# Performance work log

Hardware: AMD Instinct MI355X
Metric: run time of the kernel (lower is better)

The kernel has to match this reference:

```python
import jax, jax.numpy as jnp
import numpy as np

DIM, DEPTH, HEADS, MLP = 1024, 6, 16, 4096
HEAD_DIM = DIM // HEADS
SCALE = DIM ** -0.5  # NOTE: original uses full dim, not head_dim
EPS = 1e-5


def _layernorm(x, g, b):
    m = jnp.mean(x, axis=-1, keepdims=True)
    v = jnp.mean((x - m) ** 2, axis=-1, keepdims=True)
    return (x - m) * jax.lax.rsqrt(v + EPS) * g + b


def setup_inputs() -> dict:
    key = jax.random.key(0)
    ks = jax.random.split(key, 12)
    d = DEPTH
    s_qkv = (DIM * 3) ** -0.5  # ~kaiming-ish scale, values only need to be plausible
    inp = {
        "x": jax.random.normal(ks[0], (2, 2048, DIM), dtype=jnp.float32),
        "Wqkv": jax.random.normal(ks[1], (d, DIM, 3 * DIM), dtype=jnp.float32) * s_qkv,
        "Wout": jax.random.normal(ks[2], (d, DIM, DIM), dtype=jnp.float32) * (DIM ** -0.5),
        "bout": jnp.zeros((d, DIM), dtype=jnp.float32),
        "ln1_g": jnp.ones((d, DIM), dtype=jnp.float32),
        "ln1_b": jnp.zeros((d, DIM), dtype=jnp.float32),
        "ln2_g": jnp.ones((d, DIM), dtype=jnp.float32),
        "ln2_b": jnp.zeros((d, DIM), dtype=jnp.float32),
        "W1": jax.random.normal(ks[3], (d, DIM, MLP), dtype=jnp.float32) * (DIM ** -0.5),
        "b1": jnp.zeros((d, MLP), dtype=jnp.float32),
        "W2": jax.random.normal(ks[4], (d, MLP, DIM), dtype=jnp.float32) * (MLP ** -0.5),
        "b2": jnp.zeros((d, DIM), dtype=jnp.float32),
    }
    return inp


def _transformer(x, Wqkv, Wout, bout, ln1_g, ln1_b, ln2_g, ln2_b, W1, b1, W2, b2):
    b, n, _ = x.shape

    def layer(h, p):
        wqkv, wout, bo, g1, bb1, g2, bb2, w1, bf1, w2, bf2 = p
        # --- attention block (Residual(PreNorm(SelfAttention))) ---
        y = _layernorm(h, g1, bb1)
        qkv = y @ wqkv                                   # [b, n, 3*dim]
        qkv = qkv.reshape(b, n, 3, HEADS, HEAD_DIM)
        q, k, v = [jnp.transpose(qkv[:, :, i], (0, 2, 1, 3)) for i in range(3)]  # [b,h,n,d]
        dots = jnp.einsum("bhid,bhjd->bhij", q, k) * SCALE
        attn = jax.nn.softmax(dots, axis=-1)
        o = jnp.einsum("bhij,bhjd->bhid", attn, v)       # [b,h,n,d]
        o = jnp.transpose(o, (0, 2, 1, 3)).reshape(b, n, DIM)
        h = h + (o @ wout + bo)
        # --- FFN block (Residual(PreNorm(FeedForward))) ---
        y = _layernorm(h, g2, bb2)
        y = jax.nn.gelu(y @ w1 + bf1, approximate=False) @ w2 + bf2
        return h + y, None

    params = (Wqkv, Wout, bout, ln1_g, ln1_b, ln2_g, ln2_b, W1, b1, W2, b2)
    out, _ = jax.lax.scan(layer, x, params)
    return out


def reference(x, Wqkv, Wout, bout, ln1_g, ln1_b, ln2_g, ln2_b, W1, b1, W2, b2):
    return _transformer(x, Wqkv, Wout, bout, ln1_g, ln1_b, ln2_g, ln2_b, W1, b1, W2, b2)
```

## Files before the change

### kernel.cpp

```cpp
#include <hip/hip_runtime.h>
#include <hip/hip_bf16.h>
#include <math.h>

typedef __attribute__((__ext_vector_type__(8))) __bf16 bf16x8;
typedef __attribute__((__ext_vector_type__(4))) float f32x4;

#define DIMQ 1024
#define SEQ 2048
#define NTOK 4096
#define HEADS 16
#define HD 64
#define MLPD 4096
#define DEPTH 6

__device__ __forceinline__ void gl_lds16(const __hip_bfloat16* g, __hip_bfloat16* l) {
  __builtin_amdgcn_global_load_lds((const __attribute__((address_space(1))) void*)(g),
                                   (__attribute__((address_space(3))) void*)(l), 16, 0, 0);
}

__global__ __launch_bounds__(256) void ln_kernel(const float* __restrict__ h,
                                                 const float* __restrict__ g,
                                                 const float* __restrict__ bta,
                                                 __hip_bfloat16* __restrict__ y) {
  int row = blockIdx.x;
  int t = threadIdx.x;
  const float4* src = (const float4*)(h + (size_t)row * DIMQ);
  float4 xv = src[t];
  float s = xv.x + xv.y + xv.z + xv.w;
  float ss = xv.x * xv.x + xv.y * xv.y + xv.z * xv.z + xv.w * xv.w;
#pragma unroll
  for (int off = 32; off > 0; off >>= 1) {
    s += __shfl_xor(s, off);
    ss += __shfl_xor(ss, off);
  }
  __shared__ float red[8];
  int wid = t >> 6;
  if ((t & 63) == 0) { red[wid] = s; red[4 + wid] = ss; }
  __syncthreads();
  s = red[0] + red[1] + red[2] + red[3];
  ss = red[4] + red[5] + red[6] + red[7];
  float mean = s * (1.0f / DIMQ);
  float var = ss * (1.0f / DIMQ) - mean * mean;
  float rstd = rsqrtf(var + 1e-5f);
  float4 gv = ((const float4*)g)[t];
  float4 bv = ((const float4*)bta)[t];
  __hip_bfloat16* dst = y + (size_t)row * DIMQ + t * 4;
  dst[0] = __float2bfloat16((xv.x - mean) * rstd * gv.x + bv.x);
  dst[1] = __float2bfloat16((xv.y - mean) * rstd * gv.y + bv.y);
  dst[2] = __float2bfloat16((xv.z - mean) * rstd * gv.z + bv.z);
  dst[3] = __float2bfloat16((xv.w - mean) * rstd * gv.w + bv.w);
}

__global__ __launch_bounds__(256) void transpose_cast(const float* __restrict__ in,
                                                      __hip_bfloat16* __restrict__ out,
                                                      int K, int N) {
  __shared__ float t[32][33];
  int n0 = blockIdx.x * 32, k0 = blockIdx.y * 32;
  int tx = threadIdx.x, ty = threadIdx.y;
#pragma unroll
  for (int i = 0; i < 32; i += 8)
    t[ty + i][tx] = in[(size_t)(k0 + ty + i) * N + n0 + tx];
  __syncthreads();
#pragma unroll
  for (int i = 0; i < 32; i += 8)
    out[(size_t)(n0 + ty + i) * K + k0 + tx] = __float2bfloat16(t[tx][ty + i]);
}

__global__ __launch_bounds__(256) void vtrans(const __hip_bfloat16* __restrict__ qkvb,
                                              __hip_bfloat16* __restrict__ vT) {
  __shared__ __hip_bfloat16 t[32][33];
  int n0 = blockIdx.x * 32, d0 = blockIdx.y * 32, bh = blockIdx.z;
  int tx = threadIdx.x, ty = threadIdx.y;
#pragma unroll
  for (int i = 0; i < 32; i += 8)
    t[ty + i][tx] = qkvb[((size_t)(64 + bh) * SEQ + n0 + ty + i) * HD + d0 + tx];
  __syncthreads();
#pragma unroll
  for (int i = 0; i < 32; i += 8)
    vT[((size_t)bh * HD + d0 + ty + i) * SEQ + n0 + tx] = t[tx][ty + i];
}

template <int EPI>
__global__ __launch_bounds__(256)
void gemm128(const __hip_bfloat16* __restrict__ A, const __hip_bfloat16* __restrict__ BT,
             const float* __restrict__ bias, void* __restrict__ outp,
             int M, int N, int K, int gpx) {
  __shared__ __hip_bfloat16 As[128][64];
  __shared__ __hip_bfloat16 Bs[128][64];
  int bid = blockIdx.x;
  int xcd = bid & 7, jb = bid >> 3;
  int nt = xcd * gpx + (jb % gpx), mt = jb / gpx;
  int m0 = mt * 128, n0 = nt * 128;
  int tid = threadIdx.x;
  int lane = tid & 63, wid = tid >> 6;
  int l16 = lane & 15, quad = lane >> 4;
  int wm = (wid >> 1) * 64, wn = (wid & 1) * 64;
  int srsub = lane >> 3;
  int sg = (lane & 7) ^ srsub;
  f32x4 acc[4][4] = {};
  for (int kt = 0; kt < K; kt += 64) {
    __syncthreads();
#pragma unroll
    for (int s = 0; s < 4; ++s) {
      int r0 = (wid * 4 + s) * 8;
      gl_lds16(A + (size_t)(m0 + r0 + srsub) * K + kt + sg * 8, &As[r0][0]);
      gl_lds16(BT + (size_t)(n0 + r0 + srsub) * K + kt + sg * 8, &Bs[r0][0]);
    }
    __syncthreads();
#pragma unroll
    for (int ks = 0; ks < 2; ++ks) {
      bf16x8 af[4], bfr[4];
      int p = (ks * 4 + quad) ^ (l16 & 7);
#pragma unroll
      for (int i = 0; i < 4; ++i) af[i] = *(const bf16x8*)&As[wm + i * 16 + l16][p * 8];
#pragma unroll
      for (int j = 0; j < 4; ++j) bfr[j] = *(const bf16x8*)&Bs[wn + j * 16 + l16][p * 8];
#pragma unroll
      for (int i = 0; i < 4; ++i)
#pragma unroll
        for (int j = 0; j < 4; ++j)
          acc[i][j] = __builtin_amdgcn_mfma_f32_16x16x32_bf16(af[i], bfr[j], acc[i][j], 0, 0, 0);
    }
  }
#pragma unroll
  for (int j = 0; j < 4; ++j) {
    int col = n0 + wn + j * 16 + l16;
    float bv = (EPI == 3) ? 0.0f : bias[col];
#pragma unroll
    for (int i = 0; i < 4; ++i) {
#pragma unroll
      for (int r = 0; r < 4; ++r) {
        int row = m0 + wm + i * 16 + quad * 4 + r;
        float v = acc[i][j][r];
        if (EPI == 1) {
          v += bv;
          v = 0.5f * v * (1.0f + erff(v * 0.70710678118654752f));
          ((__hip_bfloat16*)outp)[(size_t)row * N + col] = __float2bfloat16(v);
        } else {
          int which = col >> 10;
          int head = (col >> 6) & 15;
          int d = col & 63;
          size_t dst = (((size_t)which * 32 + (row >> 11) * 16 + head) * SEQ + (row & 2047)) * HD + d;
          ((__hip_bfloat16*)outp)[dst] = __float2bfloat16(v);
        }
      }
    }
  }
}

__global__ __launch_bounds__(256, 5)
void gemm64_res(const __hip_bfloat16* __restrict__ A, const __hip_bfloat16* __restrict__ BT,
                const float* __restrict__ bias, float* __restrict__ h,
                int M, int N, int K, int gpx) {
  __shared__ __hip_bfloat16 As[128][64];
  __shared__ __hip_bfloat16 Bs[64][64];
  int bid = blockIdx.x;
  int xcd = bid & 7, jb = bid >> 3;
  int nt = xcd * gpx + (jb % gpx), mt = jb / gpx;
  int m0 = mt * 128, n0 = nt * 64;
  int tid = threadIdx.x;
  int lane = tid & 63, wid = tid >> 6;
  int l16 = lane & 15, quad = lane >> 4;
  int wm = (wid >> 1) * 64, wn = (wid & 1) * 32;
  int srsub = lane >> 3;
  int sg = (lane & 7) ^ srsub;
  f32x4 acc[4][2] = {};
  for (int kt = 0; kt < K; kt += 64) {
    __syncthreads();
#pragma unroll
    for (int s = 0; s < 4; ++s) {
      int r0 = (wid * 4 + s) * 8;
      gl_lds16(A + (size_t)(m0 + r0 + srsub) * K + kt + sg * 8, &As[r0][0]);
    }
#pragma unroll
    for (int s = 0; s < 2; ++s) {
      int r0 = (wid * 2 + s) * 8;
      gl_lds16(BT + (size_t)(n0 + r0 + srsub) * K + kt + sg * 8, &Bs[r0][0]);
    }
    __syncthreads();
#pragma unroll
    for (int ks = 0; ks < 2; ++ks) {
      bf16x8 af[4], bfr[2];
      int p = (ks * 4 + quad) ^ (l16 & 7);
#pragma unroll
      for (int i = 0; i < 4; ++i) af[i] = *(const bf16x8*)&As[wm + i * 16 + l16][p * 8];
#pragma unroll
      for (int j = 0; j < 2; ++j) bfr[j] = *(const bf16x8*)&Bs[wn + j * 16 + l16][p * 8];
#pragma unroll
      for (int i = 0; i < 4; ++i)
#pragma unroll
        for (int j = 0; j < 2; ++j)
          acc[i][j] = __builtin_amdgcn_mfma_f32_16x16x32_bf16(af[i], bfr[j], acc[i][j], 0, 0, 0);
    }
  }
#pragma unroll
  for (int j = 0; j < 2; ++j) {
    int col = n0 + wn + j * 16 + l16;
    float bv = bias[col];
#pragma unroll
    for (int i = 0; i < 4; ++i) {
#pragma unroll
      for (int r = 0; r < 4; ++r) {
        int row = m0 + wm + i * 16 + quad * 4 + r;
        size_t idx = (size_t)row * N + col;
        h[idx] = h[idx] + acc[i][j][r] + bv;
      }
    }
  }
}

__global__ __launch_bounds__(256)
void attn_kernel(const __hip_bfloat16* __restrict__ qkvb, const __hip_bfloat16* __restrict__ vT,
                 __hip_bfloat16* __restrict__ o) {
  __shared__ __hip_bfloat16 Ks[64][64];
  __shared__ __hip_bfloat16 Vs[64][64];
  __shared__ __hip_bfloat16 Ps[4][16][68];
  int bh = blockIdx.y;
  int b = bh >> 4;
  int tid = threadIdx.x;
  int wid = tid >> 6, lane = tid & 63;
  int l16 = lane & 15, quad = lane >> 4;
  int qrow = blockIdx.x * 64 + wid * 16 + l16;
  const __hip_bfloat16* qp = qkvb + ((size_t)bh * SEQ + qrow) * HD;
  bf16x8 qf0 = *(const bf16x8*)(qp + quad * 8);
  bf16x8 qf1 = *(const bf16x8*)(qp + 32 + quad * 8);
  f32x4 oacc[4] = {};
  float lsum[4] = {0.0f, 0.0f, 0.0f, 0.0f};
  int srsub = lane >> 3;
  int sg = (lane & 7) ^ srsub;
  const __hip_bfloat16* kbase = qkvb + (size_t)(32 + bh) * SEQ * HD;
  const __hip_bfloat16* vbase = vT + (size_t)bh * HD * SEQ;
  const float c1 = 0.045084220027780106f;
  for (int kb = 0; kb < SEQ; kb += 64) {
    __syncthreads();
    {
      int r0 = wid * 16, r1 = wid * 16 + 8;
      gl_lds16(kbase + (size_t)(kb + r0 + srsub) * HD + sg * 8, &Ks[r0][0]);
      gl_lds16(kbase + (size_t)(kb + r1 + srsub) * HD + sg * 8, &Ks[r1][0]);
      gl_lds16(vbase + (size_t)(r0 + srsub) * SEQ + kb + sg * 8, &Vs[r0][0]);
      gl_lds16(vbase + (size_t)(r1 + srsub) * SEQ + kb + sg * 8, &Vs[r1][0]);
    }
    __syncthreads();
    f32x4 sc[4];
    int p0 = quad ^ (l16 & 7);
    int p1 = (4 + quad) ^ (l16 & 7);
#pragma unroll
    for (int c = 0; c < 4; ++c) {
      int r = c * 16 + l16;
      bf16x8 k0 = *(const bf16x8*)&Ks[r][p0 * 8];
      bf16x8 k1 = *(const bf16x8*)&Ks[r][p1 * 8];
      f32x4 z = {};
      z = __builtin_amdgcn_mfma_f32_16x16x32_bf16(qf0, k0, z, 0, 0, 0);
      z = __builtin_amdgcn_mfma_f32_16x16x32_bf16(qf1, k1, z, 0, 0, 0);
      sc[c] = z;
    }
#pragma unroll
    for (int r = 0; r < 4; ++r) {
      float psum = 0.0f;
#pragma unroll
      for (int c = 0; c < 4; ++c) {
        float p = exp2f(sc[c][r] * c1);
        psum += p;
        Ps[wid][quad * 4 + r][c * 16 + l16] = __float2bfloat16(p);
      }
      lsum[r] += psum;
    }
    asm volatile("s_waitcnt lgkmcnt(0)" ::: "memory");
    bf16x8 pf0 = *(const bf16x8*)&Ps[wid][l16][quad * 8];
    bf16x8 pf1 = *(const bf16x8*)&Ps[wid][l16][32 + quad * 8];
#pragma unroll
    for (int f = 0; f < 4; ++f) {
      int r = f * 16 + l16;
      bf16x8 v0 = *(const bf16x8*)&Vs[r][p0 * 8];
      bf16x8 v1 = *(const bf16x8*)&Vs[r][p1 * 8];
      oacc[f] = __builtin_amdgcn_mfma_f32_16x16x32_bf16(pf0, v0, oacc[f], 0, 0, 0);
      oacc[f] = __builtin_amdgcn_mfma_f32_16x16x32_bf16(pf1, v1, oacc[f], 0, 0, 0);
    }
  }
#pragma unroll
  for (int r = 0; r < 4; ++r) {
#pragma unroll
    for (int off = 1; off < 16; off <<= 1) lsum[r] += __shfl_xor(lsum[r], off);
  }
  int h = bh & 15;
  int orow = b * SEQ + blockIdx.x * 64 + wid * 16 + quad * 4;
#pragma unroll
  for (int r = 0; r < 4; ++r) {
    float inv = 1.0f / lsum[r];
#pragma unroll
    for (int f = 0; f < 4; ++f) {
      o[(size_t)(orow + r) * DIMQ + h * HD + f * 16 + l16] = __float2bfloat16(oacc[f][r] * inv);
    }
  }
}

extern "C" void kernel_launch(void* const* d_in, const int* in_sizes, int n_in,
                              void* d_out, int out_size, void* d_ws, size_t ws_size,
                              hipStream_t stream) {
  const float* x = (const float*)d_in[0];
  const float* Wqkv = (const float*)d_in[1];
  const float* Wout = (const float*)d_in[2];
  const float* bout = (const float*)d_in[3];
  const float* ln1g = (const float*)d_in[4];
  const float* ln1b = (const float*)d_in[5];
  const float* ln2g = (const float*)d_in[6];
  const float* ln2b = (const float*)d_in[7];
  const float* W1 = (const float*)d_in[8];
  const float* b1 = (const float*)d_in[9];
  const float* W2 = (const float*)d_in[10];
  const float* b2 = (const float*)d_in[11];
  float* h = (float*)d_out;

  char* ws = (char*)d_ws;
  __hip_bfloat16* wqkvT = (__hip_bfloat16*)ws; ws += (size_t)3072 * 1024 * 2;
  __hip_bfloat16* woutT = (__hip_bfloat16*)ws; ws += (size_t)1024 * 1024 * 2;
  __hip_bfloat16* w1T = (__hip_bfloat16*)ws;   ws += (size_t)4096 * 1024 * 2;
  __hip_bfloat16* w2T = (__hip_bfloat16*)ws;   ws += (size_t)1024 * 4096 * 2;
  __hip_bfloat16* ybuf = (__hip_bfloat16*)ws;  ws += (size_t)NTOK * 1024 * 2;
  __hip_bfloat16* qkvb = (__hip_bfloat16*)ws;  ws += (size_t)NTOK * 3072 * 2;
  __hip_bfloat16* vTb = (__hip_bfloat16*)ws;   ws += (size_t)32 * HD * SEQ * 2;
  __hip_bfloat16* obuf = (__hip_bfloat16*)ws;  ws += (size_t)NTOK * 1024 * 2;
  __hip_bfloat16* actb = (__hip_bfloat16*)ws;  ws += (size_t)NTOK * MLPD * 2;

  hipMemcpyAsync(h, x, (size_t)out_size * sizeof(float), hipMemcpyDeviceToDevice, stream);

  dim3 tb(32, 8);
  for (int l = 0; l < DEPTH; ++l) {
    transpose_cast<<<dim3(3072 / 32, 1024 / 32), tb, 0, stream>>>(
        Wqkv + (size_t)l * 1024 * 3072, wqkvT, 1024, 3072);
    transpose_cast<<<dim3(1024 / 32, 1024 / 32), tb, 0, stream>>>(
        Wout + (size_t)l * 1024 * 1024, woutT, 1024, 1024);
    transpose_cast<<<dim3(4096 / 32, 1024 / 32), tb, 0, stream>>>(
        W1 + (size_t)l * 1024 * 4096, w1T, 1024, 4096);
    transpose_cast<<<dim3(1024 / 32, 4096 / 32), tb, 0, stream>>>(
        W2 + (size_t)l * 4096 * 1024, w2T, 4096, 1024);

    ln_kernel<<<NTOK, 256, 0, stream>>>(h, ln1g + l * 1024, ln1b + l * 1024, ybuf);
    gemm128<3><<<768, 256, 0, stream>>>(ybuf, wqkvT, nullptr, qkvb, NTOK, 3072, 1024, 3);
    vtrans<<<dim3(SEQ / 32, 2, 32), tb, 0, stream>>>(qkvb, vTb);
    attn_kernel<<<dim3(SEQ / 64, 32), 256, 0, stream>>>(qkvb, vTb, obuf);
    gemm64_res<<<512, 256, 0, stream>>>(obuf, woutT, bout + l * 1024, h, NTOK, 1024, 1024, 2);

    ln_kernel<<<NTOK, 256, 0, stream>>>(h, ln2g + l * 1024, ln2b + l * 1024, ybuf);
    gemm128<1><<<1024, 256, 0, stream>>>(ybuf, w1T, b1 + l * 4096, actb, NTOK, 4096, 1024, 4);
    gemm64_res<<<512, 256, 0, stream>>>(actb, w2T, b2 + l * 1024, h, NTOK, 1024, 4096, 2);
  }
}
```

Baseline: 1.932 ms.

## Double-buffer K/V tiles in attention kernel with async prefetch

Splits the attention kernel's K and V shared-memory tiles into two buffers and prefetches the next-but-one tile through direct global-to-LDS loads while the current tile is computed. Partial vmcnt waits and raw barriers replace the two full __syncthreads per iteration, so load latency can overlap the MFMA and softmax work. MFMA sections are also wrapped in s_setprio raises. This doubles the LDS used for K/V. The final iterations issue redundant wrap-around loads to keep the vmcnt count uniform, and the scheme depends on the manual waitcnt accounting being correct.

```diff
diff --git a/kernel.cpp b/kernel.cpp
--- a/kernel.cpp
+++ b/kernel.cpp
@@ -212,8 +212,8 @@
 __global__ __launch_bounds__(256)
 void attn_kernel(const __hip_bfloat16* __restrict__ qkvb, const __hip_bfloat16* __restrict__ vT,
                  __hip_bfloat16* __restrict__ o) {
-  __shared__ __hip_bfloat16 Ks[64][64];
-  __shared__ __hip_bfloat16 Vs[64][64];
+  __shared__ __hip_bfloat16 Ks[2][64][64];
+  __shared__ __hip_bfloat16 Vs[2][64][64];
   __shared__ __hip_bfloat16 Ps[4][16][68];
   int bh = blockIdx.y;
   int b = bh >> 4;
@@ -231,29 +231,38 @@
   const __hip_bfloat16* kbase = qkvb + (size_t)(32 + bh) * SEQ * HD;
   const __hip_bfloat16* vbase = vT + (size_t)bh * HD * SEQ;
   const float c1 = 0.045084220027780106f;
+
+  int r0 = wid * 16, r1 = wid * 16 + 8;
+#define STAGE_KV(bi, kb)                                                          \
+  do {                                                                            \
+    gl_lds16(kbase + (size_t)((kb) + r0 + srsub) * HD + sg * 8, &Ks[bi][r0][0]);  \
+    gl_lds16(kbase + (size_t)((kb) + r1 + srsub) * HD + sg * 8, &Ks[bi][r1][0]);  \
+    gl_lds16(vbase + (size_t)(r0 + srsub) * SEQ + (kb) + sg * 8, &Vs[bi][r0][0]); \
+    gl_lds16(vbase + (size_t)(r1 + srsub) * SEQ + (kb) + sg * 8, &Vs[bi][r1][0]); \
+  } while (0)
+
+  STAGE_KV(0, 0);
+  STAGE_KV(1, 64);
+
   for (int kb = 0; kb < SEQ; kb += 64) {
-    __syncthreads();
-    {
-      int r0 = wid * 16, r1 = wid * 16 + 8;
-      gl_lds16(kbase + (size_t)(kb + r0 + srsub) * HD + sg * 8, &Ks[r0][0]);
-      gl_lds16(kbase + (size_t)(kb + r1 + srsub) * HD + sg * 8, &Ks[r1][0]);
-      gl_lds16(vbase + (size_t)(r0 + srsub) * SEQ + kb + sg * 8, &Vs[r0][0]);
-      gl_lds16(vbase + (size_t)(r1 + srsub) * SEQ + kb + sg * 8, &Vs[r1][0]);
-    }
-    __syncthreads();
+    int cur = (kb >> 6) & 1;
+    asm volatile("s_waitcnt vmcnt(4)" ::: "memory");
+    asm volatile("s_barrier" ::: "memory");
     f32x4 sc[4];
     int p0 = quad ^ (l16 & 7);
     int p1 = (4 + quad) ^ (l16 & 7);
+    __builtin_amdgcn_s_setprio(1);
 #pragma unroll
     for (int c = 0; c < 4; ++c) {
       int r = c * 16 + l16;
-      bf16x8 k0 = *(const bf16x8*)&Ks[r][p0 * 8];
-      bf16x8 k1 = *(const bf16x8*)&Ks[r][p1 * 8];
+      bf16x8 k0 = *(const bf16x8*)&Ks[cur][r][p0 * 8];
+      bf16x8 k1 = *(const bf16x8*)&Ks[cur][r][p1 * 8];
       f32x4 z = {};
       z = __builtin_amdgcn_mfma_f32_16x16x32_bf16(qf0, k0, z, 0, 0, 0);
       z = __builtin_amdgcn_mfma_f32_16x16x32_bf16(qf1, k1, z, 0, 0, 0);
       sc[c] = z;
     }
+    __builtin_amdgcn_s_setprio(0);
 #pragma unroll
     for (int r = 0; r < 4; ++r) {
       float psum = 0.0f;
@@ -268,15 +277,23 @@
     asm volatile("s_waitcnt lgkmcnt(0)" ::: "memory");
     bf16x8 pf0 = *(const bf16x8*)&Ps[wid][l16][quad * 8];
     bf16x8 pf1 = *(const bf16x8*)&Ps[wid][l16][32 + quad * 8];
+    __builtin_amdgcn_s_setprio(1);
 #pragma unroll
     for (int f = 0; f < 4; ++f) {
       int r = f * 16 + l16;
-      bf16x8 v0 = *(const bf16x8*)&Vs[r][p0 * 8];
-      bf16x8 v1 = *(const bf16x8*)&Vs[r][p1 * 8];
+      bf16x8 v0 = *(const bf16x8*)&Vs[cur][r][p0 * 8];
+      bf16x8 v1 = *(const bf16x8*)&Vs[cur][r][p1 * 8];
       oacc[f] = __builtin_amdgcn_mfma_f32_16x16x32_bf16(pf0, v0, oacc[f], 0, 0, 0);
       oacc[f] = __builtin_amdgcn_mfma_f32_16x16x32_bf16(pf1, v1, oacc[f], 0, 0, 0);
     }
-  }
+    __builtin_amdgcn_s_setprio(0);
+    asm volatile("s_barrier" ::: "memory");
+    int nk = kb + 128;
+    if (nk >= SEQ) nk = 0;
+    STAGE_KV(cur, nk);
+  }
+#undef STAGE_KV
+
 #pragma unroll
   for (int r = 0; r < 4; ++r) {
 #pragma unroll
```

Result: slower. 2.114 ms (+9.5%).

## Fuse V transpose into QKV GEMM epilogue and merge weight transposes

Applied to the files above, without the earlier changes.

The QKV GEMM epilogue now writes the V slice directly in transposed [bh, d, seq] layout, using packed bf16 conversion and 8-byte stores, so the separate vtrans kernel and its round trip through memory are gone. The four per-layer weight transpose-cast launches are merged into one kernel that picks its source by block index, cutting launch overhead. The V epilogue writes are strided across rows of vT, which may cost some store efficiency in exchange.

```diff
diff --git a/kernel.cpp b/kernel.cpp
--- a/kernel.cpp
+++ b/kernel.cpp
@@ -16,6 +16,12 @@
 __device__ __forceinline__ void gl_lds16(const __hip_bfloat16* g, __hip_bfloat16* l) {
   __builtin_amdgcn_global_load_lds((const __attribute__((address_space(1))) void*)(g),
                                    (__attribute__((address_space(3))) void*)(l), 16, 0, 0);
+}
+
+__device__ __forceinline__ unsigned cvtpk_bf16(float lo, float hi) {
+  unsigned r;
+  asm("v_cvt_pk_bf16_f32 %0, %1, %2" : "=v"(r) : "v"(lo), "v"(hi));
+  return r;
 }
 
 __global__ __launch_bounds__(256) void ln_kernel(const float* __restrict__ h,
@@ -51,39 +57,36 @@
   dst[3] = __float2bfloat16((xv.w - mean) * rstd * gv.w + bv.w);
 }
 
-__global__ __launch_bounds__(256) void transpose_cast(const float* __restrict__ in,
-                                                      __hip_bfloat16* __restrict__ out,
-                                                      int K, int N) {
+__global__ __launch_bounds__(256)
+void transpose_cast4(const float* __restrict__ s0, const float* __restrict__ s1,
+                     const float* __restrict__ s2, const float* __restrict__ s3,
+                     __hip_bfloat16* __restrict__ d0, __hip_bfloat16* __restrict__ d1,
+                     __hip_bfloat16* __restrict__ d2, __hip_bfloat16* __restrict__ d3) {
   __shared__ float t[32][33];
-  int n0 = blockIdx.x * 32, k0 = blockIdx.y * 32;
+  int tb = blockIdx.x;
+  const float* src;
+  __hip_bfloat16* dst;
+  int K, N;
+  if (tb < 3072) { src = s0; dst = d0; K = 1024; N = 3072; }
+  else if (tb < 4096) { tb -= 3072; src = s1; dst = d1; K = 1024; N = 1024; }
+  else if (tb < 8192) { tb -= 4096; src = s2; dst = d2; K = 1024; N = 4096; }
+  else { tb -= 8192; src = s3; dst = d3; K = 4096; N = 1024; }
+  int ntx = N >> 5;
+  int n0 = (tb % ntx) * 32, k0 = (tb / ntx) * 32;
   int tx = threadIdx.x, ty = threadIdx.y;
 #pragma unroll
   for (int i = 0; i < 32; i += 8)
-    t[ty + i][tx] = in[(size_t)(k0 + ty + i) * N + n0 + tx];
+    t[ty + i][tx] = src[(size_t)(k0 + ty + i) * N + n0 + tx];
   __syncthreads();
 #pragma unroll
   for (int i = 0; i < 32; i += 8)
-    out[(size_t)(n0 + ty + i) * K + k0 + tx] = __float2bfloat16(t[tx][ty + i]);
-}
-
-__global__ __launch_bounds__(256) void vtrans(const __hip_bfloat16* __restrict__ qkvb,
-                                              __hip_bfloat16* __restrict__ vT) {
-  __shared__ __hip_bfloat16 t[32][33];
-  int n0 = blockIdx.x * 32, d0 = blockIdx.y * 32, bh = blockIdx.z;
-  int tx = threadIdx.x, ty = threadIdx.y;
-#pragma unroll
-  for (int i = 0; i < 32; i += 8)
-    t[ty + i][tx] = qkvb[((size_t)(64 + bh) * SEQ + n0 + ty + i) * HD + d0 + tx];
-  __syncthreads();
-#pragma unroll
-  for (int i = 0; i < 32; i += 8)
-    vT[((size_t)bh * HD + d0 + ty + i) * SEQ + n0 + tx] = t[tx][ty + i];
+    dst[(size_t)(n0 + ty + i) * K + k0 + tx] = __float2bfloat16(t[tx][ty + i]);
 }
 
 template <int EPI>
 __global__ __launch_bounds__(256)
 void gemm128(const __hip_bfloat16* __restrict__ A, const __hip_bfloat16* __restrict__ BT,
-             const float* __restrict__ bias, void* __restrict__ outp,
+             const float* __restrict__ bias, void* __restrict__ outp, void* __restrict__ outp2,
              int M, int N, int K, int gpx) {
   __shared__ __hip_bfloat16 As[128][64];
   __shared__ __hip_bfloat16 Bs[128][64];
@@ -125,23 +128,42 @@
 #pragma unroll
   for (int j = 0; j < 4; ++j) {
     int col = n0 + wn + j * 16 + l16;
-    float bv = (EPI == 3) ? 0.0f : bias[col];
-#pragma unroll
-    for (int i = 0; i < 4; ++i) {
-#pragma unroll
-      for (int r = 0; r < 4; ++r) {
-        int row = m0 + wm + i * 16 + quad * 4 + r;
-        float v = acc[i][j][r];
-        if (EPI == 1) {
-          v += bv;
+    if (EPI == 1) {
+      float bv = bias[col];
+#pragma unroll
+      for (int i = 0; i < 4; ++i) {
+#pragma unroll
+        for (int r = 0; r < 4; ++r) {
+          int row = m0 + wm + i * 16 + quad * 4 + r;
+          float v = acc[i][j][r] + bv;
           v = 0.5f * v * (1.0f + erff(v * 0.70710678118654752f));
           ((__hip_bfloat16*)outp)[(size_t)row * N + col] = __float2bfloat16(v);
-        } else {
-          int which = col >> 10;
-          int head = (col >> 6) & 15;
-          int d = col & 63;
-          size_t dst = (((size_t)which * 32 + (row >> 11) * 16 + head) * SEQ + (row & 2047)) * HD + d;
-          ((__hip_bfloat16*)outp)[dst] = __float2bfloat16(v);
+        }
+      }
+    } else {
+      int which = col >> 10;
+      int head = (col >> 6) & 15;
+      int d = col & 63;
+      if (which < 2) {
+#pragma unroll
+        for (int i = 0; i < 4; ++i) {
+#pragma unroll
+          for (int r = 0; r < 4; ++r) {
+            int row = m0 + wm + i * 16 + quad * 4 + r;
+            size_t dst = (((size_t)which * 32 + (row >> 11) * 16 + head) * SEQ + (row & 2047)) * HD + d;
+            ((__hip_bfloat16*)outp)[dst] = __float2bfloat16(acc[i][j][r]);
+          }
+        }
+      } else {
+        int bh2 = ((m0 >> 11) << 4) + head;
+        unsigned short* vrow = (unsigned short*)outp2 + ((size_t)bh2 * HD + d) * SEQ;
+        int nb = (m0 & 2047) + wm + quad * 4;
+#pragma unroll
+        for (int i = 0; i < 4; ++i) {
+          uint2 pk;
+          pk.x = cvtpk_bf16(acc[i][j][0], acc[i][j][1]);
+          pk.y = cvtpk_bf16(acc[i][j][2], acc[i][j][3]);
+          *(uint2*)(vrow + nb + i * 16) = pk;
         }
       }
     }
@@ -326,23 +348,18 @@
 
   dim3 tb(32, 8);
   for (int l = 0; l < DEPTH; ++l) {
-    transpose_cast<<<dim3(3072 / 32, 1024 / 32), tb, 0, stream>>>(
-        Wqkv + (size_t)l * 1024 * 3072, wqkvT, 1024, 3072);
-    transpose_cast<<<dim3(1024 / 32, 1024 / 32), tb, 0, stream>>>(
-        Wout + (size_t)l * 1024 * 1024, woutT, 1024, 1024);
-    transpose_cast<<<dim3(4096 / 32, 1024 / 32), tb, 0, stream>>>(
-        W1 + (size_t)l * 1024 * 4096, w1T, 1024, 4096);
-    transpose_cast<<<dim3(1024 / 32, 4096 / 32), tb, 0, stream>>>(
-        W2 + (size_t)l * 4096 * 1024, w2T, 4096, 1024);
+    transpose_cast4<<<12288, tb, 0, stream>>>(
+        Wqkv + (size_t)l * 1024 * 3072, Wout + (size_t)l * 1024 * 1024,
+        W1 + (size_t)l * 1024 * 4096, W2 + (size_t)l * 4096 * 1024,
+        wqkvT, woutT, w1T, w2T);
 
     ln_kernel<<<NTOK, 256, 0, stream>>>(h, ln1g + l * 1024, ln1b + l * 1024, ybuf);
-    gemm128<3><<<768, 256, 0, stream>>>(ybuf, wqkvT, nullptr, qkvb, NTOK, 3072, 1024, 3);
-    vtrans<<<dim3(SEQ / 32, 2, 32), tb, 0, stream>>>(qkvb, vTb);
+    gemm128<3><<<768, 256, 0, stream>>>(ybuf, wqkvT, nullptr, qkvb, vTb, NTOK, 3072, 1024, 3);
     attn_kernel<<<dim3(SEQ / 64, 32), 256, 0, stream>>>(qkvb, vTb, obuf);
     gemm64_res<<<512, 256, 0, stream>>>(obuf, woutT, bout + l * 1024, h, NTOK, 1024, 1024, 2);
 
     ln_kernel<<<NTOK, 256, 0, stream>>>(h, ln2g + l * 1024, ln2b + l * 1024, ybuf);
-    gemm128<1><<<1024, 256, 0, stream>>>(ybuf, w1T, b1 + l * 4096, actb, NTOK, 4096, 1024, 4);
+    gemm128<1><<<1024, 256, 0, stream>>>(ybuf, w1T, b1 + l * 4096, actb, nullptr, NTOK, 4096, 1024, 4);
     gemm64_res<<<512, 256, 0, stream>>>(actb, w2T, b2 + l * 1024, h, NTOK, 1024, 4096, 2);
   }
 }
```

New measurement: 2.010 ms. +4.1%, slower.
